# Kernel tuning notes

Measured on AMD Instinct MI355X. Metric: run time of the kernel, lower is better.

Reference implementation:

```python
import jax, jax.numpy as jnp
import numpy as np

T, B, D_IN, D_H, NQ = 512, 256, 128, 128, 8


def setup_inputs() -> dict:
    key = jax.random.key(0)
    ks = jax.random.split(key, 13)
    d_comb = D_IN + D_H
    s = 1.0 / np.sqrt(d_comb)
    inp = {
        "inputs": jax.random.normal(ks[0], (T, B, D_IN), dtype=jnp.float32),
        "Wf": jax.random.uniform(ks[1], (NQ, d_comb), jnp.float32, -s, s),
        "bf": jax.random.uniform(ks[2], (NQ,), jnp.float32, -s, s),
        "Wi": jax.random.uniform(ks[3], (NQ, d_comb), jnp.float32, -s, s),
        "bi": jax.random.uniform(ks[4], (NQ,), jnp.float32, -s, s),
        "Wu": jax.random.uniform(ks[5], (NQ, d_comb), jnp.float32, -s, s),
        "bu": jax.random.uniform(ks[6], (NQ,), jnp.float32, -s, s),
        "Wo": jax.random.uniform(ks[7], (NQ, d_comb), jnp.float32, -s, s),
        "bo": jax.random.uniform(ks[8], (NQ,), jnp.float32, -s, s),
        # trainable circuit weights (RZ angles); analytically they do not affect
        # the Z0 expectation but are kept as parameters for faithfulness.
        "qwf": jax.random.normal(ks[9], (NQ,), dtype=jnp.float32),
        "qwi": jax.random.normal(ks[10], (NQ,), dtype=jnp.float32),
        "qwu": jax.random.normal(ks[11], (NQ,), dtype=jnp.float32),
        "qwo": jax.random.normal(ks[12], (NQ,), dtype=jnp.float32),
    }
    return inp


def _qexpval(z):
    # Z0 expectation of: RX(z_i) on each qubit, RZ(w_i)+T (diagonal, drops out),
    # CNOT ring. Heisenberg: Z0 -> Z1...Z_{n-1}; <Z_j> after RX(z_j)|0> = cos(z_j).
    return jnp.prod(jnp.cos(z[:, 1:]), axis=1, keepdims=True)  # [B, 1]


def reference(inputs, Wf, bf, Wi, bi, Wu, bu, Wo, bo, qwf, qwi, qwu, qwo):
    hx = jnp.zeros((B, D_H), dtype=inputs.dtype)
    cx = jnp.zeros((B, D_H), dtype=inputs.dtype)

    def step(carry, x):
        hx, cx = carry
        c = jnp.concatenate([x, hx], axis=1)  # [B, D_IN+D_H]
        f = jax.nn.sigmoid(_qexpval(c @ Wf.T + bf))  # [B,1]
        i = jax.nn.sigmoid(_qexpval(c @ Wi.T + bi))
        g = jnp.tanh(_qexpval(c @ Wu.T + bu))
        o = jax.nn.sigmoid(_qexpval(c @ Wo.T + bo))
        cx2 = f * cx + i * g
        hx2 = o * jnp.tanh(cx2)
        return (hx2, cx2), hx2

    (hx, cx), outs = jax.lax.scan(step, (hx, cx), inputs)
    return outs, (hx, cx)
```

## Files before the change

kernel.cpp:

```cpp
#include <hip/hip_runtime.h>

#define TT 512
#define BB 256
#define DIN 128
#define DH 128
#define PFD 8

typedef __attribute__((ext_vector_type(8))) short bf16x8;
typedef __attribute__((ext_vector_type(4))) float f32x4;



__device__ __forceinline__ unsigned short f2bf(float x) {
    unsigned u = __float_as_uint(x);
    return (unsigned short)((u + 0x7fffu + ((u >> 16) & 1u)) >> 16);
}

__global__ __launch_bounds__(256) void qlstm_prep(
    const float* __restrict__ Wf, const float* __restrict__ bf,
    const float* __restrict__ Wi, const float* __restrict__ bi,
    const float* __restrict__ Wu, const float* __restrict__ bu,
    const float* __restrict__ Wo, const float* __restrict__ bo,
    float* __restrict__ swh, float* __restrict__ bias32,
    unsigned short* __restrict__ wbh, unsigned short* __restrict__ wbl)
{
    int tid = threadIdx.x;
    for (int e = tid; e < 4096; e += 256) {
        int j    = e & 7;
        int lane = (e >> 3) & 63;
        int s    = (e >> 9) & 3;
        int nt   = e >> 11;
        int n    = nt * 16 + (lane & 15);
        int k    = s * 32 + (lane >> 4) * 8 + j;
        int g    = n >> 3;
        int qi   = n & 7;
        const float* W = (g == 0) ? Wf : ((g == 1) ? Wi : ((g == 2) ? Wu : Wo));
        float val = (qi < 7) ? W[(qi + 1) * 256 + k] : 0.f;
        unsigned short h = f2bf(val);
        wbh[e] = h;
        float hf = __uint_as_float(((unsigned)h) << 16);
        wbl[e] = f2bf(val - hf);
    }
    if (tid < 32) {
        int g = tid >> 3, qi = tid & 7;
        const float* bp = (g == 0) ? bf : ((g == 1) ? bi : ((g == 2) ? bu : bo));
        bias32[tid] = (qi < 7) ? bp[qi + 1] : 0.f;
    }
    {
        int slot = tid >> 3, sfx = tid & 7;
        int g = slot >> 3, qi = slot & 7;
        const float* W = (g == 0) ? Wf : ((g == 1) ? Wi : ((g == 2) ? Wu : Wo));
        float p = 0.f;
        if (qi < 7) {
            const float* row = W + (qi + 1) * 256 + 128 + sfx * 16;
#pragma unroll
            for (int k = 0; k < 16; ++k) p += row[k];
        }
        p += __shfl_xor(p, 1);
        p += __shfl_xor(p, 2);
        p += __shfl_xor(p, 4);
        if (sfx == 0) swh[slot] = p;
    }
}

__global__ __launch_bounds__(256) void qlstm_zx(
    const float* __restrict__ X,
    const unsigned short* __restrict__ wbh,
    const unsigned short* __restrict__ wbl,
    const float* __restrict__ bias32,
    float* __restrict__ zxb)
{
    int tid  = threadIdx.x;
    int w    = tid >> 6;
    int lane = tid & 63;
    int r    = lane & 15;
    int hi   = lane >> 4;
    long rowbase = (long)blockIdx.x * 64 + w * 16;

    float b0 = bias32[r], b1 = bias32[16 + r];
    f32x4 acc0 = {b0, b0, b0, b0};
    f32x4 acc1 = {b1, b1, b1, b1};

    const float* xrow = X + (rowbase + r) * 128 + hi * 8;
#pragma unroll
    for (int s = 0; s < 4; ++s) {
        float4 xa = *(const float4*)(xrow + s * 32);
        float4 xb = *(const float4*)(xrow + s * 32 + 4);
        float xs[8] = {xa.x, xa.y, xa.z, xa.w, xb.x, xb.y, xb.z, xb.w};
        bf16x8 ah, al;
#pragma unroll
        for (int j = 0; j < 8; ++j) {
            unsigned short hh = f2bf(xs[j]);
            ah[j] = (short)hh;
            float hf = __uint_as_float(((unsigned)hh) << 16);
            al[j] = (short)f2bf(xs[j] - hf);
        }
        bf16x8 bh0 = *(const bf16x8*)(wbh + ((size_t)(0 * 4 + s) * 64 + lane) * 8);
        bf16x8 bl0 = *(const bf16x8*)(wbl + ((size_t)(0 * 4 + s) * 64 + lane) * 8);
        bf16x8 bh1 = *(const bf16x8*)(wbh + ((size_t)(1 * 4 + s) * 64 + lane) * 8);
        bf16x8 bl1 = *(const bf16x8*)(wbl + ((size_t)(1 * 4 + s) * 64 + lane) * 8);
        acc0 = __builtin_amdgcn_mfma_f32_16x16x32_bf16(ah, bh0, acc0, 0, 0, 0);
        acc0 = __builtin_amdgcn_mfma_f32_16x16x32_bf16(al, bh0, acc0, 0, 0, 0);
        acc0 = __builtin_amdgcn_mfma_f32_16x16x32_bf16(ah, bl0, acc0, 0, 0, 0);
        acc1 = __builtin_amdgcn_mfma_f32_16x16x32_bf16(ah, bh1, acc1, 0, 0, 0);
        acc1 = __builtin_amdgcn_mfma_f32_16x16x32_bf16(al, bh1, acc1, 0, 0, 0);
        acc1 = __builtin_amdgcn_mfma_f32_16x16x32_bf16(ah, bl1, acc1, 0, 0, 0);
    }
    float* zr = zxb + rowbase * 32;
#pragma unroll
    for (int reg = 0; reg < 4; ++reg) {
        int row = hi * 4 + reg;
        zr[row * 32 + r]      = acc0[reg];
        zr[row * 32 + 16 + r] = acc1[reg];
    }
}

template <int K>
__device__ __forceinline__ float quad_bcast(float v) {
    return __int_as_float(__builtin_amdgcn_mov_dpp(
        __float_as_int(v), K * 0x55, 0xf, 0xf, true));
}

__global__ __launch_bounds__(64) void qlstm_seq(
    const float* __restrict__ zxb,
    const float* __restrict__ swh,
    float* __restrict__ h_buf,
    float* __restrict__ c_buf)
{
    int lane = threadIdx.x;
    int b    = blockIdx.x * 16 + (lane >> 2);
    int g    = lane & 3;
    float4 s0 = *(const float4*)(swh + g * 8);
    float4 s1 = *(const float4*)(swh + g * 8 + 4);
    const float a    = (g == 2) ? 2.f : -1.f;
    const bool  lead = (g == 0);
    const bool  isU  = (g == 2);

    const float* pl = zxb + b * 32 + g * 8;
    float4 b0[PFD], b1[PFD];
#pragma unroll
    for (int d = 0; d < PFD; ++d) {
        b0[d] = *(const float4*)pl;
        b1[d] = *(const float4*)(pl + 4);
        pl += BB * 32;
    }

    float h = 0.f, c = 0.f;
    float* hp = h_buf + b;
    for (int tb = 0; tb < TT; tb += PFD) {
#pragma unroll
        for (int d = 0; d < PFD; ++d) {
            float4 cur0 = b0[d];
            float4 cur1 = b1[d];
            b0[d] = *(const float4*)pl;
            b1[d] = *(const float4*)(pl + 4);
            pl += BB * 32;
            float z0 = fmaf(h, s0.x, cur0.x);
            float z1 = fmaf(h, s0.y, cur0.y);
            float z2 = fmaf(h, s0.z, cur0.z);
            float z3 = fmaf(h, s0.w, cur0.w);
            float z4 = fmaf(h, s1.x, cur1.x);
            float z5 = fmaf(h, s1.y, cur1.y);
            float z6 = fmaf(h, s1.z, cur1.z);
            float q0 = __cosf(z0), q1 = __cosf(z1), q2 = __cosf(z2), q3 = __cosf(z3);
            float q4 = __cosf(z4), q5 = __cosf(z5), q6 = __cosf(z6);
            float pr = ((q0 * q1) * (q2 * q3)) * ((q4 * q5) * q6);
            float E  = __expf(a * pr);
            float rc = __builtin_amdgcn_rcpf(1.f + E);
            float val = isU ? fmaf(-2.f, rc, 1.f) : rc;
            float f_ = quad_bcast<0>(val);
            float i_ = quad_bcast<1>(val);
            float u_ = quad_bcast<2>(val);
            float o_ = quad_bcast<3>(val);
            c = fmaf(f_, c, i_ * u_);
            float E2 = __expf(2.f * c);
            float th = fmaf(-2.f, __builtin_amdgcn_rcpf(1.f + E2), 1.f);
            h = o_ * th;
            if (lead) *hp = h;
            hp += BB;
        }
    }
    if (lead) c_buf[b] = c;
}

__global__ __launch_bounds__(256) void qlstm_bcast(
    const float* __restrict__ h_buf, const float* __restrict__ c_buf,
    float4* __restrict__ out4)
{
    const int N1 = TT * BB * 32;
    const int N2 = N1 + BB * 32;
    const int N3 = N2 + BB * 32;
    int stride = gridDim.x * blockDim.x;
    for (int i = blockIdx.x * blockDim.x + threadIdx.x; i < N3; i += stride) {
        float v;
        if (i < N1)      v = h_buf[i >> 5];
        else if (i < N2) v = h_buf[(TT - 1) * BB + ((i - N1) >> 5)];
        else             v = c_buf[(i - N2) >> 5];
        out4[i] = make_float4(v, v, v, v);
    }
}

extern "C" void kernel_launch(void* const* d_in, const int* in_sizes, int n_in,
                              void* d_out, int out_size, void* d_ws, size_t ws_size,
                              hipStream_t stream)
{
    const float* X  = (const float*)d_in[0];
    const float* Wf = (const float*)d_in[1];
    const float* bf = (const float*)d_in[2];
    const float* Wi = (const float*)d_in[3];
    const float* bi = (const float*)d_in[4];
    const float* Wu = (const float*)d_in[5];
    const float* bu = (const float*)d_in[6];
    const float* Wo = (const float*)d_in[7];
    const float* bo = (const float*)d_in[8];

    float* ws    = (float*)d_ws;
    float* zxb   = ws;
    float* h_buf = ws + (size_t)TT * BB * 32;
    float* c_buf = h_buf + (size_t)TT * BB;
    float* swh   = c_buf + BB;
    float* bias32 = swh + 32;
    unsigned short* wbh = (unsigned short*)(bias32 + 32);
    unsigned short* wbl = wbh + 4096;

    qlstm_prep<<<1, 256, 0, stream>>>(Wf, bf, Wi, bi, Wu, bu, Wo, bo,
                                      swh, bias32, wbh, wbl);
    qlstm_zx<<<TT * BB / 64, 256, 0, stream>>>(X, wbh, wbl, bias32, zxb);
    qlstm_seq<<<BB / 16, 64, 0, stream>>>(zxb, swh, h_buf, c_buf);
    qlstm_bcast<<<4096, 256, 0, stream>>>(h_buf, c_buf, (float4*)d_out);
}
```

Before: 122.9 us.

## Transpose zx to batch-major, stage per-batch in LDS, fuse broadcast into sequence kernel

```diff
diff --git a/kernel.cpp b/kernel.cpp
--- a/kernel.cpp
+++ b/kernel.cpp
@@ -4,7 +4,6 @@
 #define BB 256
 #define DIN 128
 #define DH 128
-#define PFD 8
 
 typedef __attribute__((ext_vector_type(8))) short bf16x8;
 typedef __attribute__((ext_vector_type(4))) float f32x4;
@@ -68,7 +67,7 @@
     const unsigned short* __restrict__ wbh,
     const unsigned short* __restrict__ wbl,
     const float* __restrict__ bias32,
-    float* __restrict__ zxb)
+    float* __restrict__ zxbT)
 {
     int tid  = threadIdx.x;
     int w    = tid >> 6;
@@ -106,12 +105,14 @@
         acc1 = __builtin_amdgcn_mfma_f32_16x16x32_bf16(al, bh1, acc1, 0, 0, 0);
         acc1 = __builtin_amdgcn_mfma_f32_16x16x32_bf16(ah, bl1, acc1, 0, 0, 0);
     }
-    float* zr = zxb + rowbase * 32;
 #pragma unroll
     for (int reg = 0; reg < 4; ++reg) {
-        int row = hi * 4 + reg;
-        zr[row * 32 + r]      = acc0[reg];
-        zr[row * 32 + 16 + r] = acc1[reg];
+        long rowidx = rowbase + hi * 4 + reg;
+        int  bb = (int)(rowidx & 255);
+        int  tt = (int)(rowidx >> 8);
+        float* addr = zxbT + ((size_t)bb * TT + tt) * 32;
+        addr[r]      = acc0[reg];
+        addr[16 + r] = acc1[reg];
     }
 }
 
@@ -121,40 +122,45 @@
         __float_as_int(v), K * 0x55, 0xf, 0xf, true));
 }
 
-__global__ __launch_bounds__(64) void qlstm_seq(
-    const float* __restrict__ zxb,
+__global__ __launch_bounds__(256) void qlstm_seq(
+    const float* __restrict__ zxbT,
     const float* __restrict__ swh,
-    float* __restrict__ h_buf,
-    float* __restrict__ c_buf)
-{
-    int lane = threadIdx.x;
-    int b    = blockIdx.x * 16 + (lane >> 2);
-    int g    = lane & 3;
-    float4 s0 = *(const float4*)(swh + g * 8);
-    float4 s1 = *(const float4*)(swh + g * 8 + 4);
-    const float a    = (g == 2) ? 2.f : -1.f;
-    const bool  lead = (g == 0);
-    const bool  isU  = (g == 2);
-
-    const float* pl = zxb + b * 32 + g * 8;
-    float4 b0[PFD], b1[PFD];
-#pragma unroll
-    for (int d = 0; d < PFD; ++d) {
-        b0[d] = *(const float4*)pl;
-        b1[d] = *(const float4*)(pl + 4);
-        pl += BB * 32;
-    }
-
-    float h = 0.f, c = 0.f;
-    float* hp = h_buf + b;
-    for (int tb = 0; tb < TT; tb += PFD) {
-#pragma unroll
-        for (int d = 0; d < PFD; ++d) {
-            float4 cur0 = b0[d];
-            float4 cur1 = b1[d];
-            b0[d] = *(const float4*)pl;
-            b1[d] = *(const float4*)(pl + 4);
-            pl += BB * 32;
+    float* __restrict__ out)
+{
+    __shared__ float lds_z[TT * 32];
+    __shared__ float lds_h[TT];
+    __shared__ float lds_c;
+    int tid = threadIdx.x;
+    int b   = blockIdx.x;
+
+    {
+        const float4* src = (const float4*)(zxbT + (size_t)b * TT * 32);
+        float4* dst = (float4*)lds_z;
+#pragma unroll
+        for (int i = 0; i < (TT * 32 / 4) / 256; ++i)
+            dst[tid + i * 256] = src[tid + i * 256];
+    }
+    __syncthreads();
+
+    if (tid < 4) {
+        int g = tid;
+        float4 s0 = *(const float4*)(swh + g * 8);
+        float4 s1 = *(const float4*)(swh + g * 8 + 4);
+        const float a    = (g == 2) ? 2.f : -1.f;
+        const bool  lead = (g == 0);
+        const bool  isU  = (g == 2);
+
+        const float* lp0 = lds_z + g * 8;
+        float4 nx0 = *(const float4*)(lp0);
+        float4 nx1 = *(const float4*)(lp0 + 4);
+        float h = 0.f, c = 0.f;
+#pragma unroll 8
+        for (int t = 0; t < TT; ++t) {
+            float4 cur0 = nx0;
+            float4 cur1 = nx1;
+            const float* lpn = lds_z + ((t + 1) & (TT - 1)) * 32 + g * 8;
+            nx0 = *(const float4*)(lpn);
+            nx1 = *(const float4*)(lpn + 4);
             float z0 = fmaf(h, s0.x, cur0.x);
             float z1 = fmaf(h, s0.y, cur0.y);
             float z2 = fmaf(h, s0.z, cur0.z);
@@ -176,27 +182,32 @@
             float E2 = __expf(2.f * c);
             float th = fmaf(-2.f, __builtin_amdgcn_rcpf(1.f + E2), 1.f);
             h = o_ * th;
-            if (lead) *hp = h;
-            hp += BB;
-        }
-    }
-    if (lead) c_buf[b] = c;
-}
-
-__global__ __launch_bounds__(256) void qlstm_bcast(
-    const float* __restrict__ h_buf, const float* __restrict__ c_buf,
-    float4* __restrict__ out4)
-{
-    const int N1 = TT * BB * 32;
-    const int N2 = N1 + BB * 32;
-    const int N3 = N2 + BB * 32;
-    int stride = gridDim.x * blockDim.x;
-    for (int i = blockIdx.x * blockDim.x + threadIdx.x; i < N3; i += stride) {
-        float v;
-        if (i < N1)      v = h_buf[i >> 5];
-        else if (i < N2) v = h_buf[(TT - 1) * BB + ((i - N1) >> 5)];
-        else             v = c_buf[(i - N2) >> 5];
-        out4[i] = make_float4(v, v, v, v);
+            if (lead) lds_h[t] = h;
+        }
+        if (lead) lds_c = c;
+    }
+    __syncthreads();
+
+    {
+        float4* out4 = (float4*)out;
+        int tq = tid >> 5;
+        int e  = tid & 31;
+#pragma unroll 4
+        for (int t0 = 0; t0 < TT; t0 += 8) {
+            int t = t0 + tq;
+            float hv = lds_h[t];
+            float4 v = make_float4(hv, hv, hv, hv);
+            out4[((size_t)t * BB + b) * 32 + e] = v;
+        }
+        float hN = lds_h[TT - 1];
+        float cN = lds_c;
+        size_t base = (size_t)TT * BB * 32;
+        if (tid < 32) {
+            out4[base + (size_t)b * 32 + tid] = make_float4(hN, hN, hN, hN);
+        } else if (tid < 64) {
+            out4[base + (size_t)BB * 32 + (size_t)b * 32 + (tid - 32)] =
+                make_float4(cN, cN, cN, cN);
+        }
     }
 }
 
@@ -214,18 +225,15 @@
     const float* Wo = (const float*)d_in[7];
     const float* bo = (const float*)d_in[8];
 
-    float* ws    = (float*)d_ws;
-    float* zxb   = ws;
-    float* h_buf = ws + (size_t)TT * BB * 32;
-    float* c_buf = h_buf + (size_t)TT * BB;
-    float* swh   = c_buf + BB;
+    float* ws     = (float*)d_ws;
+    float* zxbT   = ws;
+    float* swh    = ws + (size_t)BB * TT * 32;
     float* bias32 = swh + 32;
     unsigned short* wbh = (unsigned short*)(bias32 + 32);
     unsigned short* wbl = wbh + 4096;
 
     qlstm_prep<<<1, 256, 0, stream>>>(Wf, bf, Wi, bi, Wu, bu, Wo, bo,
                                       swh, bias32, wbh, wbl);
-    qlstm_zx<<<TT * BB / 64, 256, 0, stream>>>(X, wbh, wbl, bias32, zxb);
-    qlstm_seq<<<BB / 16, 64, 0, stream>>>(zxb, swh, h_buf, c_buf);
-    qlstm_bcast<<<4096, 256, 0, stream>>>(h_buf, c_buf, (float4*)d_out);
-}
+    qlstm_zx<<<TT * BB / 64, 256, 0, stream>>>(X, wbh, wbl, bias32, zxbT);
+    qlstm_seq<<<BB, 256, 0, stream>>>(zxbT, swh, (float*)d_out);
+}
```

After: 136.2 us. +10.7%, slower.
